# Kernel tuning notes

Hardware: AMD Instinct MI355X
Metric: run time of the kernel (lower is better)

The kernel has to match this reference:

```python
import jax, jax.numpy as jnp
import numpy as np

# Hyperparameters (from __init__ defaults)
TIME_RES = 25
BASE_RES = 512
MAX_RES = 32768
N_LEVELS = 8
N_FEATS = 4
LOG2_HASHMAP = 13
HASHMAP_SIZE = 1 << LOG2_HASHMAP  # 8192
PRIME_Y = np.uint32(2654435761)   # instant-ngp 2D hash prime (dim0 prime is 1)

# Per-level grid scales (tcnn convention: scale = 2^(l*log2_pls)*base - 1)
_LOG2_PLS = np.log2(MAX_RES / BASE_RES) / (N_LEVELS - 1)
SCALES = jnp.asarray(np.exp2(np.arange(N_LEVELS) * _LOG2_PLS) * BASE_RES - 1.0,
                     dtype=jnp.float32)  # [L]


def _hash_encode(x, table_t):
    """Instant-NGP 2D multires hash encoding for one time slice.
    x: [N,2] in [0,1); table_t: [L, H, F]. Returns [N, L*F].
    All levels satisfy res^2 > HASHMAP_SIZE, so always the hash path."""
    N = x.shape[0]
    pos = x[:, None, :] * SCALES[None, :, None] + 0.5        # [N,L,2]
    pos_i = jnp.floor(pos)
    frac = pos - pos_i                                        # [N,L,2]
    pos_i = pos_i.astype(jnp.uint32)
    lvl = jnp.arange(N_LEVELS, dtype=jnp.int32)[None, :]      # [1,L]
    acc = jnp.zeros((N, N_LEVELS, N_FEATS), dtype=table_t.dtype)
    mask = jnp.uint32(HASHMAP_SIZE - 1)
    for dx in (0, 1):  # 4 bilinear corners (static unroll)
        for dy in (0, 1):
            ix = pos_i[..., 0] + jnp.uint32(dx)               # [N,L]
            iy = pos_i[..., 1] + jnp.uint32(dy)
            h = jnp.bitwise_xor(ix, iy * PRIME_Y) & mask      # [N,L] hash index
            w = (frac[..., 0] if dx else 1.0 - frac[..., 0]) * \
                (frac[..., 1] if dy else 1.0 - frac[..., 1])  # [N,L]
            f = table_t[lvl, h.astype(jnp.int32)]             # [N,L,F] gather
            acc = acc + w[..., None] * f
    return acc.reshape(N, N_LEVELS * N_FEATS)


def setup_inputs() -> dict:
    key = jax.random.key(0)
    k1, k2 = jax.random.split(key)
    N = 2_000_000
    x = jax.random.uniform(k1, (N, 2), dtype=jnp.float32)
    t = jnp.asarray(0.3, dtype=jnp.float32)  # scalar time in [0,1]
    # tcnn initializes hash tables uniform in [-1e-4, 1e-4]
    table = jax.random.uniform(k2, (TIME_RES, N_LEVELS, HASHMAP_SIZE, N_FEATS),
                               dtype=jnp.float32, minval=-1e-4, maxval=1e-4)
    return {"x": x, "t": t, "table": table}


def reference(x, t, table):
    idx = t * (TIME_RES - 1)
    i1 = jnp.floor(idx).astype(jnp.int32)
    i2 = jnp.ceil(idx).astype(jnp.int32)
    # blend weight; equals (i2-idx, idx-i1) when i1!=i2 and (1,0) when equal,
    # matching the torch branch semantics.
    w2 = idx - i1.astype(idx.dtype)
    w1 = 1.0 - w2
    tab1 = jax.lax.dynamic_index_in_dim(table, i1, axis=0, keepdims=False)
    tab2 = jax.lax.dynamic_index_in_dim(table, i2, axis=0, keepdims=False)
    f1 = _hash_encode(x, tab1)  # [N, 32]
    f2 = _hash_encode(x, tab2)
    return w1 * f1 + w2 * f2
```

## Files before the change

kernel.cpp:

```cpp
#include <hip/hip_runtime.h>
#include <hip/hip_fp16.h>
#include <math.h>

#define NLV 8
#define NF 4
#define HSZ 8192
#define TRES 25
#define PRIME 2654435761u

struct Scales { float s[NLV]; };

__global__ __launch_bounds__(256) void blend_kernel(
    const float* __restrict__ table, const float* __restrict__ tptr,
    __half2* __restrict__ bt)
{
    int i = blockIdx.x * 256 + threadIdx.x;
    float t = *tptr;
    float idx = t * (float)(TRES - 1);
    float fi1 = floorf(idx);
    float fi2 = ceilf(idx);
    float w2 = idx - fi1;
    float w1 = 1.0f - w2;
    size_t off1 = (size_t)(int)fi1 * (size_t)(NLV * HSZ * NF);
    size_t off2 = (size_t)(int)fi2 * (size_t)(NLV * HSZ * NF);
    float4 a = ((const float4*)(table + off1))[i];
    float4 b = ((const float4*)(table + off2))[i];
    float4 r;
    r.x = w1 * a.x + w2 * b.x;
    r.y = w1 * a.y + w2 * b.y;
    r.z = w1 * a.z + w2 * b.z;
    r.w = w1 * a.w + w2 * b.w;
    bt[2 * (size_t)i]     = __floats2half2_rn(r.x, r.y);
    bt[2 * (size_t)i + 1] = __floats2half2_rn(r.z, r.w);
}

__device__ __forceinline__ float2 h2f(unsigned u) {
    return __half22float2(__builtin_bit_cast(__half2, u));
}

__device__ __forceinline__ float4 gather_lvl(const uint2* tbl, float2 p, float scale)
{
    float px = __fadd_rn(__fmul_rn(p.x, scale), 0.5f);
    float py = __fadd_rn(__fmul_rn(p.y, scale), 0.5f);
    float fx0 = floorf(px), fy0 = floorf(py);
    float fx = px - fx0, fy = py - fy0;
    unsigned ix = (unsigned)(int)fx0;
    unsigned iy = (unsigned)(int)fy0;
    unsigned hy0 = iy * PRIME;
    unsigned hy1 = hy0 + PRIME;
    unsigned h00 = (ix         ^ hy0) & (HSZ - 1);
    unsigned h01 = (ix         ^ hy1) & (HSZ - 1);
    unsigned h10 = ((ix + 1u)  ^ hy0) & (HSZ - 1);
    unsigned h11 = ((ix + 1u)  ^ hy1) & (HSZ - 1);
    uint2 v00 = tbl[h00];
    uint2 v01 = tbl[h01];
    uint2 v10 = tbl[h10];
    uint2 v11 = tbl[h11];
    float gx = 1.0f - fx, gy = 1.0f - fy;
    float w00 = gx * gy, w01 = gx * fy, w10 = fx * gy, w11 = fx * fy;
    float2 a00 = h2f(v00.x), b00 = h2f(v00.y);
    float2 a01 = h2f(v01.x), b01 = h2f(v01.y);
    float2 a10 = h2f(v10.x), b10 = h2f(v10.y);
    float2 a11 = h2f(v11.x), b11 = h2f(v11.y);
    float4 r;
    r.x = w00 * a00.x + w01 * a01.x + w10 * a10.x + w11 * a11.x;
    r.y = w00 * a00.y + w01 * a01.y + w10 * a10.y + w11 * a11.y;
    r.z = w00 * b00.x + w01 * b01.x + w10 * b10.x + w11 * b11.x;
    r.w = w00 * b00.y + w01 * b01.y + w10 * b10.y + w11 * b11.y;
    return r;
}

__device__ __forceinline__ void stage_dma(const float4* __restrict__ src,
                                          float4* dst, int tid)
{
    #pragma unroll
    for (int k = 0; k < 4; ++k) {
        __builtin_amdgcn_global_load_lds(
            (const __attribute__((address_space(1))) unsigned int*)(src + tid + k * 1024),
            (__attribute__((address_space(3))) unsigned int*)(dst + tid + k * 1024),
            16, 0, 0);
    }
}

__global__ __launch_bounds__(1024)
__attribute__((amdgpu_waves_per_eu(4, 4)))
void encode_kernel(
    const float* __restrict__ x, const float4* __restrict__ bt,
    float* __restrict__ out, int npts, Scales sc)
{
    __shared__ float4 smem[2][4096];
    int tid = threadIdx.x;
    int n0 = blockIdx.x * 1024 + tid;
    int c0 = n0 < npts ? n0 : npts - 1;
    float2 p = ((const float2*)x)[c0];

    stage_dma(bt, smem[0], tid);

    float4 a0, a1, a2, a3, a4, a5, a6, a7;

#define PHASE(L, ACC)                                                        \
    {                                                                        \
        if ((L) < NLV - 1)                                                   \
            stage_dma(bt + (size_t)((L) + 1) * 4096, smem[((L) + 1) & 1], tid);\
        if ((L) < NLV - 1) asm volatile("s_waitcnt vmcnt(4)" ::: "memory");  \
        else               asm volatile("s_waitcnt vmcnt(0)" ::: "memory");  \
        __builtin_amdgcn_s_barrier();                                        \
        __builtin_amdgcn_sched_barrier(0);                                   \
        ACC = gather_lvl((const uint2*)smem[(L) & 1], p, sc.s[(L)]);         \
        if ((L) < NLV - 1) {                                                 \
            __builtin_amdgcn_sched_barrier(0);                               \
            __builtin_amdgcn_s_barrier();                                    \
        }                                                                    \
    }

    PHASE(0, a0)
    PHASE(1, a1)
    PHASE(2, a2)
    PHASE(3, a3)
    PHASE(4, a4)
    PHASE(5, a5)
    PHASE(6, a6)
    PHASE(7, a7)
#undef PHASE

    if (n0 < npts) {
        float4* o = (float4*)(out + (size_t)n0 * 32);
        o[0] = a0; o[1] = a1; o[2] = a2; o[3] = a3;
        o[4] = a4; o[5] = a5; o[6] = a6; o[7] = a7;
    }
}

extern "C" void kernel_launch(void* const* d_in, const int* in_sizes, int n_in,
                              void* d_out, int out_size, void* d_ws, size_t ws_size,
                              hipStream_t stream) {
    const float* x     = (const float*)d_in[0];
    const float* t     = (const float*)d_in[1];
    const float* table = (const float*)d_in[2];
    float* out = (float*)d_out;
    __half2* bt = (__half2*)d_ws;

    int npts = in_sizes[0] / 2;

    Scales sc;
    const double l2p = log2(32768.0 / 512.0) / 7.0;
    for (int l = 0; l < NLV; ++l)
        sc.s[l] = (float)(exp2((double)l * l2p) * 512.0 - 1.0);

    blend_kernel<<<(NLV * HSZ) / 256, 256, 0, stream>>>(table, t, bt);

    int nblocks = (npts + 1023) / 1024;
    encode_kernel<<<nblocks, 1024, 0, stream>>>(
        x, (const float4*)bt, out, npts, sc);
}
```

Baseline: 369.8 us.

## Process two points per thread to amortize per-level table staging

Result: slower. 419.4 us (+13.4%).

```diff
diff --git a/kernel.cpp b/kernel.cpp
--- a/kernel.cpp
+++ b/kernel.cpp
@@ -90,15 +90,19 @@
 {
     __shared__ float4 smem[2][4096];
     int tid = threadIdx.x;
-    int n0 = blockIdx.x * 1024 + tid;
+    int base = blockIdx.x * 2048 + tid;
+    int n0 = base, n1 = base + 1024;
     int c0 = n0 < npts ? n0 : npts - 1;
-    float2 p = ((const float2*)x)[c0];
+    int c1 = n1 < npts ? n1 : npts - 1;
+    float2 p0 = ((const float2*)x)[c0];
+    float2 p1 = ((const float2*)x)[c1];
 
     stage_dma(bt, smem[0], tid);
 
     float4 a0, a1, a2, a3, a4, a5, a6, a7;
+    float4 b0, b1, b2, b3, b4, b5, b6, b7;
 
-#define PHASE(L, ACC)                                                        \
+#define PHASE(L, A, B)                                                       \
     {                                                                        \
         if ((L) < NLV - 1)                                                   \
             stage_dma(bt + (size_t)((L) + 1) * 4096, smem[((L) + 1) & 1], tid);\
@@ -106,27 +110,37 @@
         else               asm volatile("s_waitcnt vmcnt(0)" ::: "memory");  \
         __builtin_amdgcn_s_barrier();                                        \
         __builtin_amdgcn_sched_barrier(0);                                   \
-        ACC = gather_lvl((const uint2*)smem[(L) & 1], p, sc.s[(L)]);         \
+        {                                                                    \
+            const uint2* tbl = (const uint2*)smem[(L) & 1];                  \
+            float s = sc.s[(L)];                                             \
+            A = gather_lvl(tbl, p0, s);                                      \
+            B = gather_lvl(tbl, p1, s);                                      \
+        }                                                                    \
         if ((L) < NLV - 1) {                                                 \
             __builtin_amdgcn_sched_barrier(0);                               \
             __builtin_amdgcn_s_barrier();                                    \
         }                                                                    \
     }
 
-    PHASE(0, a0)
-    PHASE(1, a1)
-    PHASE(2, a2)
-    PHASE(3, a3)
-    PHASE(4, a4)
-    PHASE(5, a5)
-    PHASE(6, a6)
-    PHASE(7, a7)
+    PHASE(0, a0, b0)
+    PHASE(1, a1, b1)
+    PHASE(2, a2, b2)
+    PHASE(3, a3, b3)
+    PHASE(4, a4, b4)
+    PHASE(5, a5, b5)
+    PHASE(6, a6, b6)
+    PHASE(7, a7, b7)
 #undef PHASE
 
     if (n0 < npts) {
         float4* o = (float4*)(out + (size_t)n0 * 32);
         o[0] = a0; o[1] = a1; o[2] = a2; o[3] = a3;
         o[4] = a4; o[5] = a5; o[6] = a6; o[7] = a7;
+    }
+    if (n1 < npts) {
+        float4* o = (float4*)(out + (size_t)n1 * 32);
+        o[0] = b0; o[1] = b1; o[2] = b2; o[3] = b3;
+        o[4] = b4; o[5] = b5; o[6] = b6; o[7] = b7;
     }
 }
 
@@ -148,7 +162,7 @@
 
     blend_kernel<<<(NLV * HSZ) / 256, 256, 0, stream>>>(table, t, bt);
 
-    int nblocks = (npts + 1023) / 1024;
+    int nblocks = (npts + 2047) / 2048;
     encode_kernel<<<nblocks, 1024, 0, stream>>>(
         x, (const float4*)bt, out, npts, sc);
 }
```
